# Kernel tuning notes

Measured on AMD Instinct MI355X. Metric: run time of the kernel, lower is better.

The kernel has to match this reference:

```python
import jax, jax.numpy as jnp
import numpy as np
import math

HEADS = 16
MAX_LEN = 512  # tokens; seq must equal this for the relative bias to be valid
D_HEAD = 64
BH = 256  # batch*heads


def setup_inputs() -> dict:
    key = jax.random.key(0)
    k1, k2, k3, k4 = jax.random.split(key, 4)
    S, B, D = MAX_LEN, BH, D_HEAD
    return {
        "query": jax.random.normal(k1, (S, B, D), dtype=jnp.float32),
        "key": jax.random.normal(k2, (S, B, D), dtype=jnp.float32),
        "value": jax.random.normal(k3, (S, B, D), dtype=jnp.float32),
        # per-head relative position embedding table [heads, 2*tokens-1, d_head]
        "k_rpos_emb": jax.random.normal(k4, (HEADS, 2 * MAX_LEN - 1, D), dtype=jnp.float32),
    }


def reference(query, key, value, k_rpos_emb):
    # 'seq b f -> b seq f'
    q = jnp.transpose(query, (1, 0, 2))   # [bh, s, d]
    k = jnp.transpose(key, (1, 0, 2))
    v = jnp.transpose(value, (1, 0, 2))
    bh, s, d = q.shape
    b = bh // HEADS

    # relative position bias from keys: split heads, contract with per-head table
    kh = k.reshape(b, HEADS, s, d)                                   # [b,h,s,d]
    rel_logits = jnp.einsum('bhid,hrd->bhir', kh, k_rpos_emb)        # [b,h,s,2L-1]
    rel_idx = (jnp.arange(s)[None, :] - jnp.arange(s)[:, None]
               + MAX_LEN - 1).astype(jnp.int32)                      # [s,s] in [0,2L-2]
    rel_bias = jnp.take_along_axis(
        rel_logits, rel_idx[None, None, :, :], axis=-1)              # [b,h,s,s]
    rel_bias = rel_bias.reshape(bh, s, s)

    scale = 1.0 / math.sqrt(d)
    scores = (jnp.einsum('bid,bjd->bij', q, k) + rel_bias) * scale   # [bh,s,s]
    attn = jax.nn.softmax(scores, axis=-1)
    out = jnp.einsum('bij,bjd->bid', attn, v)                        # [bh,s,d]
    return jnp.transpose(out, (1, 0, 2))                             # [s,bh,d]
```

## Files before the change

### kernel.cpp

```cpp
#include <hip/hip_runtime.h>
#include <hip/hip_bf16.h>

#define S_LEN  512
#define D_DIM  64
#define NH     16
#define R_LEN  1023
#define BHD    16384
#define PPITCH 68
#define SCL2   0.1803368801111204f

typedef __attribute__((ext_vector_type(8))) short   short8_t;
typedef __attribute__((ext_vector_type(8))) __bf16  bf16x8;
typedef __attribute__((ext_vector_type(4))) float   floatx4;

__device__ __forceinline__ unsigned short f2bf(float f) {
  union { float f; unsigned u; } v; v.f = f;
  return (unsigned short)((v.u + 0x7fffu + ((v.u >> 16) & 1u)) >> 16);
}
__device__ __forceinline__ ushort2 c2(float x, float y) {
  __hip_bfloat162 h = __float22bfloat162_rn(float2{x, y});
  union { __hip_bfloat162 h; ushort2 u; } v; v.h = h; return v.u;
}
__device__ __forceinline__ short8_t pack8s(float4 a, float4 b) {
  union { ushort2 u2[4]; short8_t s8; } u;
  u.u2[0] = c2(a.x, a.y); u.u2[1] = c2(a.z, a.w);
  u.u2[2] = c2(b.x, b.y); u.u2[3] = c2(b.z, b.w);
  return u.s8;
}
__device__ __forceinline__ bf16x8 pack8(float4 a, float4 b) {
  short8_t s = pack8s(a, b);
  return __builtin_bit_cast(bf16x8, s);
}
__device__ __forceinline__ bf16x8 ldfrag(const unsigned short* p) {
  short8_t s = *(const short8_t*)p;
  return __builtin_bit_cast(bf16x8, s);
}
__device__ __forceinline__ bf16x8 ldfrag8(const unsigned short* p) {
  union { ushort4 u4[2]; short8_t s8; } u;
  u.u4[0] = *(const ushort4*)p;
  u.u4[1] = *(const ushort4*)(p + 4);
  return __builtin_bit_cast(bf16x8, u.s8);
}
__device__ __forceinline__ bf16x8 ldseg(const unsigned short* buf, int r, int seg) {
  return ldfrag(buf + r * 64 + ((seg ^ (r & 7)) << 3));
}
__device__ __forceinline__ void async16(const void* g, void* l) {
  __builtin_amdgcn_global_load_lds(
      (const __attribute__((address_space(1))) unsigned int*)(unsigned long long)(uintptr_t)g,
      (__attribute__((address_space(3))) unsigned int*)(unsigned int)(uintptr_t)l,
      16, 0, 0);
}
__device__ __forceinline__ void stage16(const unsigned short* gb, size_t rstride,
                                        unsigned short* lb, int lane) {
  int srow = lane >> 3;
  int sseg = (lane & 7) ^ srow;
  async16(gb + (size_t)srow * rstride + sseg * 8, lb);
  async16(gb + (size_t)(srow + 8) * rstride + sseg * 8, lb + 512);
}
__device__ __forceinline__ void stageE(const unsigned short* gb, int sigma,
                                       unsigned short* slot, int lane, int wv) {
  int srow = lane >> 3;
  int sseg = (lane & 7) ^ srow;
  int r0 = sigma * 64 + wv * 16 + srow;
  unsigned short* lb = slot + (wv * 16) * 64;
  async16(gb + (size_t)min(r0, R_LEN - 1) * D_DIM + sseg * 8, lb);
  async16(gb + (size_t)min(r0 + 8, R_LEN - 1) * D_DIM + sseg * 8, lb + 512);
}
template<int N>
__device__ __forceinline__ float dpp_ror(float x) {
  int i = __builtin_bit_cast(int, x);
  int r = __builtin_amdgcn_update_dpp(i, i, 0x120 + N, 0xF, 0xF, false);
  return __builtin_bit_cast(float, r);
}
__device__ __forceinline__ float rmax16(float x) {
  x = fmaxf(x, dpp_ror<8>(x)); x = fmaxf(x, dpp_ror<4>(x));
  x = fmaxf(x, dpp_ror<2>(x)); x = fmaxf(x, dpp_ror<1>(x));
  return x;
}
__device__ __forceinline__ float rsum16(float x) {
  x += dpp_ror<8>(x); x += dpp_ror<4>(x);
  x += dpp_ror<2>(x); x += dpp_ror<1>(x);
  return x;
}
__device__ __forceinline__ float fexp2(float x) {
#if __has_builtin(__builtin_amdgcn_exp2f)
  return __builtin_amdgcn_exp2f(x);
#else
  return exp2f(x);
#endif
}

extern "C" __global__ void prepass(const float* __restrict__ k, const float* __restrict__ v,
                                   const float* __restrict__ emb,
                                   unsigned short* __restrict__ kb,
                                   unsigned short* __restrict__ vtb,
                                   unsigned short* __restrict__ eb) {
  __shared__ unsigned short t[64 * PPITCH];
  const int bid = blockIdx.x;
  const int tid = threadIdx.x;
  if (bid < 4096) {
    size_t i = (size_t)bid * 256 + tid;
    const float* s = k + i * 8;
    float4 a = *(const float4*)s, b = *(const float4*)(s + 4);
    *(short8_t*)(kb + i * 8) = pack8s(a, b);
  } else if (bid < 4608) {
    size_t i = (size_t)(bid - 4096) * 256 + tid;
    if (i < 130944) {
      const float* s = emb + i * 8;
      float4 a = *(const float4*)s, b = *(const float4*)(s + 4);
      *(short8_t*)(eb + i * 8) = pack8s(a, b);
    }
  } else {
    const int b2 = bid - 4608;
    const int bh = b2 >> 3;
    const int j0 = (b2 & 7) << 6;
    for (int idx = tid; idx < 1024; idx += 256) {
      int jl = idx >> 4, cg = (idx & 15) << 2;
      float4 a = *(const float4*)(v + (size_t)(j0 + jl) * BHD + bh * D_DIM + cg);
      ushort2 u0 = c2(a.x, a.y), u1 = c2(a.z, a.w);
      *(ushort4*)(t + jl * PPITCH + cg) = (ushort4){ u0.x, u0.y, u1.x, u1.y };
    }
    __syncthreads();
    for (int slot = tid; slot < 512; slot += 256) {
      int d = slot >> 3, jseg = slot & 7;
      union { unsigned short u[8]; short8_t s8; } r;
      #pragma unroll
      for (int jj = 0; jj < 8; ++jj) r.u[jj] = t[(jseg * 8 + jj) * PPITCH + d];
      *(short8_t*)(vtb + ((size_t)bh * D_DIM + d) * S_LEN + j0 + jseg * 8) = r.s8;
    }
  }
}

extern "C" __global__ __launch_bounds__(256, 2)
void attn_relbias(const float* __restrict__ q, const unsigned short* __restrict__ kb,
                  const unsigned short* __restrict__ vtb,
                  const unsigned short* __restrict__ eb,
                  float* __restrict__ out)
{
  __shared__ unsigned short kbuf[2][4096];
  __shared__ unsigned short vbuf[2][4096];
  __shared__ unsigned short ebuf[4][4096];
  __shared__ unsigned short ps[4][16 * PPITCH];

  const int tid  = threadIdx.x;
  const int bh   = blockIdx.x & 255;
  const int i0   = (blockIdx.x >> 8) << 7;
  const int h    = bh & (NH - 1);
  const int wv   = tid >> 6;
  const int lane = tid & 63;
  const int l15  = lane & 15;
  const int quad = lane >> 4;
  const int iloc0 = wv * 16 + quad * 4;
  const int elo   = 3 - wv;
  const int arow  = wv * 16 + l15;
  const int acol  = quad * 8;
  const int it0   = 7 - (i0 >> 6);

  const unsigned short* kgb  = kb  + (size_t)bh * D_DIM;
  const unsigned short* vgb  = vtb + (size_t)bh * (D_DIM * S_LEN);
  const unsigned short* egb  = eb  + (size_t)h * (R_LEN * D_DIM);

  stage16(kgb + (size_t)(wv * 16) * BHD, BHD, &kbuf[0][(wv * 16) * 64], lane);
  stage16(vgb + (size_t)(wv * 16) * S_LEN, S_LEN, &vbuf[0][(wv * 16) * 64], lane);
  stageE(egb, it0 - 1, ebuf[(it0 - 1) & 3], lane, wv);
  stageE(egb, it0,     ebuf[it0 & 3],       lane, wv);
  stageE(egb, it0 + 1, ebuf[(it0 + 1) & 3], lane, wv);

  bf16x8 qa0[2], qa1[2], ia0[2], ia1[2];
  #pragma unroll
  for (int st = 0; st < 2; ++st) {
    const int row = i0 + st * 64 + arow;
    const float* gq = q + (size_t)row * BHD + bh * D_DIM + acol;
    qa0[st] = pack8(*(const float4*)gq,        *(const float4*)(gq + 4));
    qa1[st] = pack8(*(const float4*)(gq + 32), *(const float4*)(gq + 36));
    const unsigned short* gi = kb + (size_t)row * BHD + bh * D_DIM + acol;
    ia0[st] = ldfrag(gi);
    ia1[st] = ldfrag(gi + 32);
  }

  floatx4 oacc[2][4];
  float m_i[2][4], l_i[2][4];
  #pragma unroll
  for (int st = 0; st < 2; ++st) {
    #pragma unroll
    for (int r = 0; r < 4; ++r) {
      oacc[st][r] = (floatx4){0.f, 0.f, 0.f, 0.f};
      m_i[st][r] = -1e30f; l_i[st][r] = 0.f;
    }
  }

  __syncthreads();

  #pragma unroll 2
  for (int t = 0; t < 8; ++t) {
    if (t < 7) {
      const int j1 = t * 64 + 64;
      stage16(kgb + (size_t)(j1 + wv * 16) * BHD, BHD, &kbuf[(t + 1) & 1][(wv * 16) * 64], lane);
      stage16(vgb + (size_t)(wv * 16) * S_LEN + j1, S_LEN, &vbuf[(t + 1) & 1][(wv * 16) * 64], lane);
      stageE(egb, it0 + t + 2, ebuf[(it0 + t + 2) & 3], lane, wv);
    }
    const unsigned short* kc = kbuf[t & 1];
    const unsigned short* vc = vbuf[t & 1];

    floatx4 bacc[2][5];
    #pragma unroll
    for (int st = 0; st < 2; ++st) {
      const int sbase = it0 - st + t;
      #pragma unroll
      for (int ei = 0; ei < 5; ++ei) {
        const int eblk = elo + ei;
        const unsigned short* es = ebuf[(sbase + (eblk >> 2)) & 3];
        const int lr = (eblk * 16 + l15) & 63;
        floatx4 bz = (floatx4){0.f, 0.f, 0.f, 0.f};
        bz = __builtin_amdgcn_mfma_f32_16x16x32_bf16(ia0[st], ldseg(es, lr, quad),     bz, 0, 0, 0);
        bz = __builtin_amdgcn_mfma_f32_16x16x32_bf16(ia1[st], ldseg(es, lr, quad + 4), bz, 0, 0, 0);
        bacc[st][ei] = bz;
      }
    }

    floatx4 qk[2][4];
    #pragma unroll
    for (int c = 0; c < 4; ++c) {
      bf16x8 k0 = ldseg(kc, c * 16 + l15, quad);
      bf16x8 k1 = ldseg(kc, c * 16 + l15, quad + 4);
      #pragma unroll
      for (int st = 0; st < 2; ++st) {
        floatx4 acc = (floatx4){0.f, 0.f, 0.f, 0.f};
        acc = __builtin_amdgcn_mfma_f32_16x16x32_bf16(qa0[st], k0, acc, 0, 0, 0);
        acc = __builtin_amdgcn_mfma_f32_16x16x32_bf16(qa1[st], k1, acc, 0, 0, 0);
        qk[st][c] = acc;
      }
    }

    float p[2][4][4];
    #pragma unroll
    for (int st = 0; st < 2; ++st) {
      float sc[4][4];
      #pragma unroll
      for (int r = 0; r < 4; ++r) {
        const int o  = 15 - 4 * quad - r;
        const int ls = (lane & 48) + ((l15 + o) & 15);
        const bool hi = (l15 + o) >= 16;
        #pragma unroll
        for (int c = 0; c < 4; ++c) {
          float blo = __shfl(bacc[st][c][r],     ls);
          float bhi = __shfl(bacc[st][c + 1][r], ls);
          sc[c][r] = (qk[st][c][r] + (hi ? bhi : blo)) * SCL2;
        }
      }
      #pragma unroll
      for (int r = 0; r < 4; ++r) {
        float mx = fmaxf(fmaxf(sc[0][r], sc[1][r]), fmaxf(sc[2][r], sc[3][r]));
        mx = rmax16(mx);
        float mnew  = fmaxf(m_i[st][r], mx);
        float alpha = fexp2(m_i[st][r] - mnew);
        float rs = 0.f;
        #pragma unroll
        for (int c = 0; c < 4; ++c) { p[st][c][r] = fexp2(sc[c][r] - mnew); rs += p[st][c][r]; }
        rs = rsum16(rs);
        l_i[st][r] = l_i[st][r] * alpha + rs;
        m_i[st][r] = mnew;
        #pragma unroll
        for (int c = 0; c < 4; ++c) oacc[st][c][r] *= alpha;
      }
    }

    unsigned short* psw = ps[wv];
    bf16x8 vb0[4], vb1[4];
    {
      #pragma unroll
      for (int r = 0; r < 4; ++r) {
        ushort2 u01 = c2(p[0][0][r], p[0][1][r]);
        ushort2 u23 = c2(p[0][2][r], p[0][3][r]);
        unsigned short* pr = psw + (quad * 4 + r) * PPITCH + l15;
        pr[0]  = u01.x; pr[16] = u01.y; pr[32] = u23.x; pr[48] = u23.y;
      }
      bf16x8 pa0 = ldfrag8(psw + l15 * PPITCH + acol);
      bf16x8 pa1 = ldfrag8(psw + l15 * PPITCH + acol + 32);
      #pragma unroll
      for (int c = 0; c < 4; ++c) {
        vb0[c] = ldseg(vc, c * 16 + l15, quad);
        vb1[c] = ldseg(vc, c * 16 + l15, quad + 4);
        oacc[0][c] = __builtin_amdgcn_mfma_f32_16x16x32_bf16(pa0, vb0[c], oacc[0][c], 0, 0, 0);
        oacc[0][c] = __builtin_amdgcn_mfma_f32_16x16x32_bf16(pa1, vb1[c], oacc[0][c], 0, 0, 0);
      }
    }
    {
      #pragma unroll
      for (int r = 0; r < 4; ++r) {
        ushort2 u01 = c2(p[1][0][r], p[1][1][r]);
        ushort2 u23 = c2(p[1][2][r], p[1][3][r]);
        unsigned short* pr = psw + (quad * 4 + r) * PPITCH + l15;
        pr[0]  = u01.x; pr[16] = u01.y; pr[32] = u23.x; pr[48] = u23.y;
      }
      bf16x8 pa0 = ldfrag8(psw + l15 * PPITCH + acol);
      bf16x8 pa1 = ldfrag8(psw + l15 * PPITCH + acol + 32);
      #pragma unroll
      for (int c = 0; c < 4; ++c) {
        oacc[1][c] = __builtin_amdgcn_mfma_f32_16x16x32_bf16(pa0, vb0[c], oacc[1][c], 0, 0, 0);
        oacc[1][c] = __builtin_amdgcn_mfma_f32_16x16x32_bf16(pa1, vb1[c], oacc[1][c], 0, 0, 0);
      }
    }

    __syncthreads();
  }

  #pragma unroll
  for (int st = 0; st < 2; ++st) {
    #pragma unroll
    for (int r = 0; r < 4; ++r) {
      float inv = 1.f / l_i[st][r];
      int row = i0 + st * 64 + iloc0 + r;
      #pragma unroll
      for (int c = 0; c < 4; ++c)
        out[(size_t)row * BHD + bh * D_DIM + c * 16 + l15] = oacc[st][c][r] * inv;
    }
  }
}

#define PITCH 72
extern "C" __global__ __launch_bounds__(256, 4)
void attn_fb(const float* __restrict__ q, const float* __restrict__ k,
             const float* __restrict__ v, const float* __restrict__ emb,
             float* __restrict__ out)
{
  __shared__ unsigned short kjs[64 * PITCH];
  __shared__ unsigned short vts[64 * PITCH];
  __shared__ unsigned short ps2[4][16 * PPITCH];

  const int tid  = threadIdx.x;
  const int bh   = blockIdx.x >> 3;
  const int i0   = (blockIdx.x & 7) << 6;
  const int h    = bh & (NH - 1);
  const int wv   = tid >> 6;
  const int lane = tid & 63;
  const int l15  = lane & 15;
  const int quad = lane >> 4;
  const int iloc0 = wv * 16 + quad * 4;
  const int elo   = 3 - wv;

  {
    const float* gq = q + (size_t)i0 * BHD + bh * D_DIM;
    const float* gk = k + (size_t)i0 * BHD + bh * D_DIM;
    for (int idx = tid; idx < 1024; idx += 256) {
      int row = idx >> 4, cg = (idx & 15) << 2;
      float4 a = *(const float4*)(gq + row * BHD + cg);
      float4 b = *(const float4*)(gk + row * BHD + cg);
      *(ushort4*)(vts + row * PITCH + cg) = (ushort4){ f2bf(a.x), f2bf(a.y), f2bf(a.z), f2bf(a.w) };
      *(ushort4*)(kjs + row * PITCH + cg) = (ushort4){ f2bf(b.x), f2bf(b.y), f2bf(b.z), f2bf(b.w) };
    }
  }
  __syncthreads();

  const int arow = wv * 16 + l15;
  const int acol = quad * 8;
  bf16x8 qa0 = ldfrag(vts + arow * PITCH + acol);
  bf16x8 qa1 = ldfrag(vts + arow * PITCH + acol + 32);
  bf16x8 ia0 = ldfrag(kjs + arow * PITCH + acol);
  bf16x8 ia1 = ldfrag(kjs + arow * PITCH + acol + 32);

  floatx4 oacc[4];
  #pragma unroll
  for (int c = 0; c < 4; ++c) oacc[c] = (floatx4){0.f, 0.f, 0.f, 0.f};
  float m_i[4] = { -1e30f, -1e30f, -1e30f, -1e30f };
  float l_i[4] = { 0.f, 0.f, 0.f, 0.f };

  for (int j0 = 0; j0 < S_LEN; j0 += 64) {
    __syncthreads();
    {
      const float* gk = k + (size_t)j0 * BHD + bh * D_DIM;
      for (int idx = tid; idx < 1024; idx += 256) {
        int row = idx >> 4, cg = (idx & 15) << 2;
        float4 b = *(const float4*)(gk + row * BHD + cg);
        *(ushort4*)(kjs + row * PITCH + cg) = (ushort4){ f2bf(b.x), f2bf(b.y), f2bf(b.z), f2bf(b.w) };
      }
    }
    {
      const float* gv = v + (size_t)j0 * BHD + bh * D_DIM;
      for (int idx = tid; idx < 1024; idx += 256) {
        int dg = idx & 15, jl = idx >> 4;
        float4 b = *(const float4*)(gv + jl * BHD + dg * 4);
        int d0 = dg * 4;
        vts[(d0 + 0) * PITCH + jl] = f2bf(b.x);
        vts[(d0 + 1) * PITCH + jl] = f2bf(b.y);
        vts[(d0 + 2) * PITCH + jl] = f2bf(b.z);
        vts[(d0 + 3) * PITCH + jl] = f2bf(b.w);
      }
    }
    floatx4 bacc[5];
    {
      const int rbase = j0 - i0 + 448;
      #pragma unroll
      for (int ei = 0; ei < 5; ++ei) {
        int rg = rbase + (elo + ei) * 16 + l15;
        rg = min(rg, R_LEN - 1);
        const float* ep = emb + ((size_t)h * R_LEN + rg) * D_DIM + acol;
        float4 e0 = *(const float4*)(ep);
        float4 e1 = *(const float4*)(ep + 4);
        float4 e2 = *(const float4*)(ep + 32);
        float4 e3 = *(const float4*)(ep + 36);
        floatx4 bz = (floatx4){0.f, 0.f, 0.f, 0.f};
        bz = __builtin_amdgcn_mfma_f32_16x16x32_bf16(ia0, pack8(e0, e1), bz, 0, 0, 0);
        bz = __builtin_amdgcn_mfma_f32_16x16x32_bf16(ia1, pack8(e2, e3), bz, 0, 0, 0);
        bacc[ei] = bz;
      }
    }
    __syncthreads();

    floatx4 qk[4];
    #pragma unroll
    for (int c = 0; c < 4; ++c) {
      bf16x8 kb0 = ldfrag(kjs + (c * 16 + l15) * PITCH + acol);
      bf16x8 kb1 = ldfrag(kjs + (c * 16 + l15) * PITCH + acol + 32);
      floatx4 acc = (floatx4){0.f, 0.f, 0.f, 0.f};
      acc = __builtin_amdgcn_mfma_f32_16x16x32_bf16(qa0, kb0, acc, 0, 0, 0);
      acc = __builtin_amdgcn_mfma_f32_16x16x32_bf16(qa1, kb1, acc, 0, 0, 0);
      qk[c] = acc;
    }
    float sc[4][4];
    #pragma unroll
    for (int r = 0; r < 4; ++r) {
      const int o  = 15 - 4 * quad - r;
      const int ls = (lane & 48) + ((l15 + o) & 15);
      const bool hi = (l15 + o) >= 16;
      #pragma unroll
      for (int c = 0; c < 4; ++c) {
        float blo = __shfl(bacc[c][r],     ls);
        float bhi = __shfl(bacc[c + 1][r], ls);
        sc[c][r] = (qk[c][r] + (hi ? bhi : blo)) * 0.125f;
      }
    }
    float p[4][4];
    #pragma unroll
    for (int r = 0; r < 4; ++r) {
      float mx = fmaxf(fmaxf(sc[0][r], sc[1][r]), fmaxf(sc[2][r], sc[3][r]));
      mx = rmax16(mx);
      float mnew  = fmaxf(m_i[r], mx);
      float alpha = __expf(m_i[r] - mnew);
      float rs = 0.f;
      #pragma unroll
      for (int c = 0; c < 4; ++c) { p[c][r] = __expf(sc[c][r] - mnew); rs += p[c][r]; }
      rs = rsum16(rs);
      l_i[r] = l_i[r] * alpha + rs;
      m_i[r] = mnew;
      #pragma unroll
      for (int c = 0; c < 4; ++c) oacc[c][r] *= alpha;
    }
    unsigned short* psw = ps2[wv];
    #pragma unroll
    for (int c = 0; c < 4; ++c) {
      #pragma unroll
      for (int r = 0; r < 4; ++r)
        psw[(quad * 4 + r) * PPITCH + c * 16 + l15] = f2bf(p[c][r]);
    }
    bf16x8 pa0 = ldfrag8(psw + l15 * PPITCH + acol);
    bf16x8 pa1 = ldfrag8(psw + l15 * PPITCH + acol + 32);
    #pragma unroll
    for (int c = 0; c < 4; ++c) {
      bf16x8 vb0 = ldfrag(vts + (c * 16 + l15) * PITCH + acol);
      bf16x8 vb1 = ldfrag(vts + (c * 16 + l15) * PITCH + acol + 32);
      oacc[c] = __builtin_amdgcn_mfma_f32_16x16x32_bf16(pa0, vb0, oacc[c], 0, 0, 0);
      oacc[c] = __builtin_amdgcn_mfma_f32_16x16x32_bf16(pa1, vb1, oacc[c], 0, 0, 0);
    }
  }
  #pragma unroll
  for (int r = 0; r < 4; ++r) {
    float inv = 1.f / l_i[r];
    int row = i0 + iloc0 + r;
    #pragma unroll
    for (int c = 0; c < 4; ++c)
      out[(size_t)row * BHD + bh * D_DIM + c * 16 + l15] = oacc[c][r] * inv;
  }
}

extern "C" void kernel_launch(void* const* d_in, const int* in_sizes, int n_in,
                              void* d_out, int out_size, void* d_ws, size_t ws_size,
                              hipStream_t stream) {
  const float* q   = (const float*)d_in[0];
  const float* k   = (const float*)d_in[1];
  const float* v   = (const float*)d_in[2];
  const float* emb = (const float*)d_in[3];
  float* out = (float*)d_out;

  const size_t kb_off  = 0;
  const size_t vtb_off = (size_t)512 * 256 * 64 * 2;
  const size_t eb_off  = vtb_off * 2;
  const size_t need    = eb_off + (size_t)NH * R_LEN * D_DIM * 2;

  if (ws_size >= need) {
    unsigned short* kbp  = (unsigned short*)((char*)d_ws + kb_off);
    unsigned short* vtbp = (unsigned short*)((char*)d_ws + vtb_off);
    unsigned short* ebp  = (unsigned short*)((char*)d_ws + eb_off);
    hipLaunchKernelGGL(prepass, dim3(6656), dim3(256), 0, stream, k, v, emb, kbp, vtbp, ebp);
    hipLaunchKernelGGL(attn_relbias, dim3(1024), dim3(256), 0, stream,
                       q, kbp, vtbp, ebp, out);
  } else {
    hipLaunchKernelGGL(attn_fb, dim3(2048), dim3(256), 0, stream, q, k, v, emb, out);
  }
}
```

Baseline: 201.5 us.

## Prescale Q and embeddings, add lazy softmax rescale, and set MFMA priority

Folds the softmax scale (log2e/sqrt(d)) into Q during packing and into the relative-position embedding table in the prepass, which removes the per-score multiply. Adds a conditional rescale: when every row max in the wavefront grows by no more than a threshold, the old running max is kept and the alpha rescale of the accumulator is skipped, which saves exp and multiply work. Raises wave priority around the MFMA blocks with s_setprio so matrix work from different waves interleaves better. Extra bf16 rounding after scaling slightly changes numerics, and the lazy max lets unnormalized values grow by up to 2^8.

```diff
diff --git a/kernel.cpp b/kernel.cpp
--- a/kernel.cpp
+++ b/kernel.cpp
@@ -8,6 +8,7 @@
 #define BHD    16384
 #define PPITCH 68
 #define SCL2   0.1803368801111204f
+#define DTHR   8.0f
 
 typedef __attribute__((ext_vector_type(8))) short   short8_t;
 typedef __attribute__((ext_vector_type(8))) __bf16  bf16x8;
@@ -30,6 +31,11 @@
 __device__ __forceinline__ bf16x8 pack8(float4 a, float4 b) {
   short8_t s = pack8s(a, b);
   return __builtin_bit_cast(bf16x8, s);
+}
+__device__ __forceinline__ bf16x8 pack8scaled(float4 a, float4 b, float s) {
+  a.x *= s; a.y *= s; a.z *= s; a.w *= s;
+  b.x *= s; b.y *= s; b.z *= s; b.w *= s;
+  return pack8(a, b);
 }
 __device__ __forceinline__ bf16x8 ldfrag(const unsigned short* p) {
   short8_t s = *(const short8_t*)p;
@@ -108,7 +114,8 @@
     if (i < 130944) {
       const float* s = emb + i * 8;
       float4 a = *(const float4*)s, b = *(const float4*)(s + 4);
-      *(short8_t*)(eb + i * 8) = pack8s(a, b);
+      bf16x8 r = pack8scaled(a, b, SCL2);
+      *(short8_t*)(eb + i * 8) = __builtin_bit_cast(short8_t, r);
     }
   } else {
     const int b2 = bid - 4608;
@@ -171,8 +178,8 @@
   for (int st = 0; st < 2; ++st) {
     const int row = i0 + st * 64 + arow;
     const float* gq = q + (size_t)row * BHD + bh * D_DIM + acol;
-    qa0[st] = pack8(*(const float4*)gq,        *(const float4*)(gq + 4));
-    qa1[st] = pack8(*(const float4*)(gq + 32), *(const float4*)(gq + 36));
+    qa0[st] = pack8scaled(*(const float4*)gq,        *(const float4*)(gq + 4), SCL2);
+    qa1[st] = pack8scaled(*(const float4*)(gq + 32), *(const float4*)(gq + 36), SCL2);
     const unsigned short* gi = kb + (size_t)row * BHD + bh * D_DIM + acol;
     ia0[st] = ldfrag(gi);
     ia1[st] = ldfrag(gi + 32);
@@ -203,6 +210,8 @@
     const unsigned short* vc = vbuf[t & 1];
 
     floatx4 bacc[2][5];
+    floatx4 qk[2][4];
+    __builtin_amdgcn_s_setprio(1);
     #pragma unroll
     for (int st = 0; st < 2; ++st) {
       const int sbase = it0 - st + t;
@@ -217,8 +226,6 @@
         bacc[st][ei] = bz;
       }
     }
-
-    floatx4 qk[2][4];
     #pragma unroll
     for (int c = 0; c < 4; ++c) {
       bf16x8 k0 = ldseg(kc, c * 16 + l15, quad);
@@ -231,8 +238,10 @@
         qk[st][c] = acc;
       }
     }
-
-    float p[2][4][4];
+    __builtin_amdgcn_s_setprio(0);
+
+    unsigned short* psw = ps[wv];
+    bf16x8 vb0[4], vb1[4];
     #pragma unroll
     for (int st = 0; st < 2; ++st) {
       float sc[4][4];
@@ -245,61 +254,62 @@
         for (int c = 0; c < 4; ++c) {
           float blo = __shfl(bacc[st][c][r],     ls);
           float bhi = __shfl(bacc[st][c + 1][r], ls);
-          sc[c][r] = (qk[st][c][r] + (hi ? bhi : blo)) * SCL2;
+          sc[c][r] = qk[st][c][r] + (hi ? bhi : blo);
         }
       }
+      float mx4[4];
       #pragma unroll
       for (int r = 0; r < 4; ++r) {
         float mx = fmaxf(fmaxf(sc[0][r], sc[1][r]), fmaxf(sc[2][r], sc[3][r]));
-        mx = rmax16(mx);
-        float mnew  = fmaxf(m_i[st][r], mx);
-        float alpha = fexp2(m_i[st][r] - mnew);
-        float rs = 0.f;
+        mx4[r] = rmax16(mx);
+      }
+      float dm = fmaxf(fmaxf(mx4[0] - m_i[st][0], mx4[1] - m_i[st][1]),
+                       fmaxf(mx4[2] - m_i[st][2], mx4[3] - m_i[st][3]));
+      float p[4][4];
+      if (__all(dm <= DTHR)) {
         #pragma unroll
-        for (int c = 0; c < 4; ++c) { p[st][c][r] = fexp2(sc[c][r] - mnew); rs += p[st][c][r]; }
-        rs = rsum16(rs);
-        l_i[st][r] = l_i[st][r] * alpha + rs;
-        m_i[st][r] = mnew;
+        for (int r = 0; r < 4; ++r) {
+          float rs = 0.f;
+          #pragma unroll
+          for (int c = 0; c < 4; ++c) { p[c][r] = fexp2(sc[c][r] - m_i[st][r]); rs += p[c][r]; }
+          rs = rsum16(rs);
+          l_i[st][r] += rs;
+        }
+      } else {
         #pragma unroll
-        for (int c = 0; c < 4; ++c) oacc[st][c][r] *= alpha;
-      }
-    }
-
-    unsigned short* psw = ps[wv];
-    bf16x8 vb0[4], vb1[4];
-    {
+        for (int r = 0; r < 4; ++r) {
+          float mnew  = fmaxf(m_i[st][r], mx4[r]);
+          float alpha = fexp2(m_i[st][r] - mnew);
+          float rs = 0.f;
+          #pragma unroll
+          for (int c = 0; c < 4; ++c) { p[c][r] = fexp2(sc[c][r] - mnew); rs += p[c][r]; }
+          rs = rsum16(rs);
+          l_i[st][r] = l_i[st][r] * alpha + rs;
+          m_i[st][r] = mnew;
+          #pragma unroll
+          for (int c = 0; c < 4; ++c) oacc[st][c][r] *= alpha;
+        }
+      }
       #pragma unroll
       for (int r = 0; r < 4; ++r) {
-        ushort2 u01 = c2(p[0][0][r], p[0][1][r]);
-        ushort2 u23 = c2(p[0][2][r], p[0][3][r]);
+        ushort2 u01 = c2(p[0][r], p[1][r]);
+        ushort2 u23 = c2(p[2][r], p[3][r]);
         unsigned short* pr = psw + (quad * 4 + r) * PPITCH + l15;
         pr[0]  = u01.x; pr[16] = u01.y; pr[32] = u23.x; pr[48] = u23.y;
       }
       bf16x8 pa0 = ldfrag8(psw + l15 * PPITCH + acol);
       bf16x8 pa1 = ldfrag8(psw + l15 * PPITCH + acol + 32);
+      __builtin_amdgcn_s_setprio(1);
       #pragma unroll
       for (int c = 0; c < 4; ++c) {
-        vb0[c] = ldseg(vc, c * 16 + l15, quad);
-        vb1[c] = ldseg(vc, c * 16 + l15, quad + 4);
-        oacc[0][c] = __builtin_amdgcn_mfma_f32_16x16x32_bf16(pa0, vb0[c], oacc[0][c], 0, 0, 0);
-        oacc[0][c] = __builtin_amdgcn_mfma_f32_16x16x32_bf16(pa1, vb1[c], oacc[0][c], 0, 0, 0);
-      }
-    }
-    {
-      #pragma unroll
-      for (int r = 0; r < 4; ++r) {
-        ushort2 u01 = c2(p[1][0][r], p[1][1][r]);
-        ushort2 u23 = c2(p[1][2][r], p[1][3][r]);
-        unsigned short* pr = psw + (quad * 4 + r) * PPITCH + l15;
-        pr[0]  = u01.x; pr[16] = u01.y; pr[32] = u23.x; pr[48] = u23.y;
-      }
-      bf16x8 pa0 = ldfrag8(psw + l15 * PPITCH + acol);
-      bf16x8 pa1 = ldfrag8(psw + l15 * PPITCH + acol + 32);
-      #pragma unroll
-      for (int c = 0; c < 4; ++c) {
-        oacc[1][c] = __builtin_amdgcn_mfma_f32_16x16x32_bf16(pa0, vb0[c], oacc[1][c], 0, 0, 0);
-        oacc[1][c] = __builtin_amdgcn_mfma_f32_16x16x32_bf16(pa1, vb1[c], oacc[1][c], 0, 0, 0);
-      }
+        if (st == 0) {
+          vb0[c] = ldseg(vc, c * 16 + l15, quad);
+          vb1[c] = ldseg(vc, c * 16 + l15, quad + 4);
+        }
+        oacc[st][c] = __builtin_amdgcn_mfma_f32_16x16x32_bf16(pa0, vb0[c], oacc[st][c], 0, 0, 0);
+        oacc[st][c] = __builtin_amdgcn_mfma_f32_16x16x32_bf16(pa1, vb1[c], oacc[st][c], 0, 0, 0);
+      }
+      __builtin_amdgcn_s_setprio(0);
     }
 
     __syncthreads();
```

New measurement: 201.6 us. Within noise of the previous version (+0.0%).
